# Optimization experiments

Hardware: AMD Instinct MI355X
Metric: run time of the kernel (lower is better)

The kernel has to match this reference:

```python
import jax, jax.numpy as jnp
import numpy as np

N_ATOMS = 100000
N_EDGES = 800000
ATOM_FDIM = 133
HIDDEN = 256
DEPTH = 3
NUM_MOLS = 4096
BN_EPS = 1e-5


def setup_inputs() -> dict:
    key = jax.random.key(0)
    ks = jax.random.split(key, 16)
    f_atoms = jax.random.normal(ks[0], (N_ATOMS, ATOM_FDIM), dtype=jnp.float32)
    edge_index = jax.random.randint(ks[1], (2, N_EDGES), 0, N_ATOMS, dtype=jnp.int64)
    segment_ids = jnp.sort(jax.random.randint(ks[2], (N_ATOMS,), 0, NUM_MOLS, dtype=jnp.int64))
    s = 1.0 / np.sqrt(HIDDEN)
    return {
        "f_atoms": f_atoms,
        "W_in_w": jax.random.normal(ks[3], (ATOM_FDIM, HIDDEN), dtype=jnp.float32) / np.sqrt(ATOM_FDIM),
        "W_in_b": jnp.zeros((HIDDEN,), dtype=jnp.float32),
        "w1": jax.random.normal(ks[4], (DEPTH, HIDDEN, HIDDEN), dtype=jnp.float32) * s,
        "b1": jnp.zeros((DEPTH, HIDDEN), dtype=jnp.float32),
        "g1": jnp.ones((DEPTH, HIDDEN), dtype=jnp.float32),
        "be1": jnp.zeros((DEPTH, HIDDEN), dtype=jnp.float32),
        "w2": jax.random.normal(ks[5], (DEPTH, HIDDEN, HIDDEN), dtype=jnp.float32) * s,
        "b2": jnp.zeros((DEPTH, HIDDEN), dtype=jnp.float32),
        "g2": jnp.ones((DEPTH, HIDDEN), dtype=jnp.float32),
        "be2": jnp.zeros((DEPTH, HIDDEN), dtype=jnp.float32),
        "eps": jnp.zeros((DEPTH,), dtype=jnp.float32),
        "edge_index": edge_index,
        "segment_ids": segment_ids,
    }


def batchnorm(h, gamma, beta):
    # BatchNorm1d with batch statistics over the node dimension (training-mode math)
    mean = jnp.mean(h, axis=0)
    var = jnp.var(h, axis=0)
    return (h - mean) * jax.lax.rsqrt(var + BN_EPS) * gamma + beta


def reference(f_atoms, W_in_w, W_in_b, w1, b1, g1, be1, w2, b2, g2, be2, eps,
              edge_index, segment_ids):
    src, dst = edge_index[0], edge_index[1]
    x = jax.nn.relu(f_atoms @ W_in_w + W_in_b)  # [N, H]
    for i in range(DEPTH):
        agg = jnp.zeros_like(x).at[dst].add(x[src])  # gather + scatter-add
        h = agg + (1.0 + eps[i]) * x                 # epsilon self-term
        h = jax.nn.relu(batchnorm(h @ w1[i] + b1[i], g1[i], be1[i]))
        h = jax.nn.relu(batchnorm(h @ w2[i] + b2[i], g2[i], be2[i]))
        x = h  # dropout = identity (eval)
    sums = jax.ops.segment_sum(x, segment_ids, num_segments=NUM_MOLS)
    counts = jax.ops.segment_sum(jnp.ones((x.shape[0],), x.dtype), segment_ids,
                                 num_segments=NUM_MOLS)
    return sums / jnp.maximum(counts, 1.0)[:, None]  # per-molecule mean
```

## Files before the change

kernel.cpp:

```cpp
#include <hip/hip_runtime.h>
#include <hip/hip_bf16.h>

#define NA 100000
#define NE 800000
#define FDIM 133
#define KIN 192
#define H 256
#define NMOL 4096

typedef __attribute__((ext_vector_type(8))) short s16x8;
typedef __attribute__((ext_vector_type(4))) float f32x4;
typedef __attribute__((ext_vector_type(4))) unsigned short u16x4;

__device__ __forceinline__ float bf2f(unsigned short h) {
    unsigned u = ((unsigned)h) << 16;
    return __builtin_bit_cast(float, u);
}
__device__ __forceinline__ unsigned short f2bf(float f) {
    unsigned u = __builtin_bit_cast(unsigned, f);
    u = u + 0x7FFFu + ((u >> 16) & 1u);
    return (unsigned short)(u >> 16);
}

__device__ __forceinline__ int swz(int row, int g) {
    return row * 64 + ((g ^ (row & 7)) << 3);
}

template<bool A_F32, bool AFFINE, bool RELU_OUT, bool STATS>
__global__ __launch_bounds__(256) void gemm_k(
    const void* __restrict__ Avoid,
    const unsigned short* __restrict__ BT,
    const float* __restrict__ bias,
    const float* __restrict__ aSc, const float* __restrict__ aSh,
    unsigned short* __restrict__ C,
    float* __restrict__ stSum, float* __restrict__ stSq,
    int M, int Kpad)
{
    __shared__ short lsA[128 * 64];
    __shared__ short lsB[128 * 64];
    __shared__ float lsSc[256], lsSh[256];
    __shared__ float lsS[128], lsQ[128];

    const int t = threadIdx.x;
    const int m0 = blockIdx.y * 128;
    const int n0 = blockIdx.x * 128;

    if (STATS && t < 128) { lsS[t] = 0.f; lsQ[t] = 0.f; }
    if (AFFINE) { lsSc[t] = aSc[t]; lsSh[t] = aSh[t]; }
    if (AFFINE) __syncthreads();

    const int sr = t >> 3;
    const int sg = t & 7;
    const int lane = t & 63;
    const int wid = t >> 6;
    const int wm = wid >> 1, wn = wid & 1;
    const int fr = lane & 15, fg = lane >> 4;

    f32x4 acc[4][4];
    #pragma unroll
    for (int i = 0; i < 4; i++)
        #pragma unroll
        for (int j = 0; j < 4; j++)
            acc[i][j] = f32x4{0.f, 0.f, 0.f, 0.f};

    const int nK = Kpad >> 6;
    s16x8 ra[4], rb[4];

    auto loadRegs = [&](int kc) {
        const int k0 = kc * 64;
        #pragma unroll
        for (int p = 0; p < 4; ++p) {
            int r = p * 32 + sr;
            int ga = m0 + r;
            if (A_F32) {
                const float* Af = (const float*)Avoid;
                s16x8 v;
                #pragma unroll
                for (int e = 0; e < 8; ++e) {
                    int k = k0 + sg * 8 + e;
                    float f = (ga < M && k < FDIM) ? Af[(size_t)ga * FDIM + k] : 0.f;
                    v[e] = (short)f2bf(f);
                }
                ra[p] = v;
            } else {
                const unsigned short* A = (const unsigned short*)Avoid;
                s16x8 z = {0,0,0,0,0,0,0,0};
                ra[p] = (ga < M) ? *(const s16x8*)(A + (size_t)ga * Kpad + k0 + sg * 8) : z;
            }
            rb[p] = *(const s16x8*)(BT + (size_t)(n0 + p * 32 + sr) * Kpad + k0 + sg * 8);
        }
    };
    auto writeLds = [&](int kc) {
        const int k0 = kc * 64;
        #pragma unroll
        for (int p = 0; p < 4; ++p) {
            int r = p * 32 + sr;
            s16x8 va = ra[p];
            if (AFFINE) {
                #pragma unroll
                for (int e = 0; e < 8; ++e) {
                    int k = k0 + sg * 8 + e;
                    float f = bf2f((unsigned short)va[e]);
                    f = fmaxf(f * lsSc[k] + lsSh[k], 0.f);
                    va[e] = (short)f2bf(f);
                }
            }
            *(s16x8*)&lsA[swz(r, sg)] = va;
            *(s16x8*)&lsB[swz(r, sg)] = rb[p];
        }
    };

    loadRegs(0);
    for (int kc = 0; kc < nK; ++kc) {
        writeLds(kc);
        __syncthreads();
        if (kc + 1 < nK) loadRegs(kc + 1);
        #pragma unroll
        for (int ks = 0; ks < 2; ++ks) {
            s16x8 af[4], bg[4];
            #pragma unroll
            for (int mi = 0; mi < 4; ++mi)
                af[mi] = *(const s16x8*)&lsA[swz(wm * 64 + mi * 16 + fr, ks * 4 + fg)];
            #pragma unroll
            for (int ni = 0; ni < 4; ++ni)
                bg[ni] = *(const s16x8*)&lsB[swz(wn * 64 + ni * 16 + fr, ks * 4 + fg)];
            #pragma unroll
            for (int mi = 0; mi < 4; ++mi)
                #pragma unroll
                for (int ni = 0; ni < 4; ++ni)
                    acc[mi][ni] = __builtin_amdgcn_mfma_f32_16x16x32_bf16(
                        af[mi], bg[ni], acc[mi][ni], 0, 0, 0);
        }
        __syncthreads();
    }

    float bc[4];
    #pragma unroll
    for (int ni = 0; ni < 4; ++ni)
        bc[ni] = bias[n0 + wn * 64 + ni * 16 + fr];
    float cs[4] = {0.f, 0.f, 0.f, 0.f}, cq[4] = {0.f, 0.f, 0.f, 0.f};
    #pragma unroll
    for (int mi = 0; mi < 4; ++mi) {
        #pragma unroll
        for (int r = 0; r < 4; ++r) {
            int row = m0 + wm * 64 + mi * 16 + fg * 4 + r;
            if (row < M) {
                #pragma unroll
                for (int ni = 0; ni < 4; ++ni) {
                    float v = acc[mi][ni][r] + bc[ni];
                    if (RELU_OUT) v = fmaxf(v, 0.f);
                    if (STATS) { cs[ni] += v; cq[ni] += v * v; }
                    C[(size_t)row * H + n0 + wn * 64 + ni * 16 + fr] = f2bf(v);
                }
            }
        }
    }
    if (STATS) {
        #pragma unroll
        for (int ni = 0; ni < 4; ++ni) {
            atomicAdd(&lsS[wn * 64 + ni * 16 + fr], cs[ni]);
            atomicAdd(&lsQ[wn * 64 + ni * 16 + fr], cq[ni]);
        }
        __syncthreads();
        if (t < 128) {
            atomicAdd(&stSum[n0 + t], lsS[t]);
            atomicAdd(&stSq[n0 + t], lsQ[t]);
        }
    }
}

__global__ void bnfin_k(float* __restrict__ sum, float* __restrict__ sumsq,
                        const float* __restrict__ g, const float* __restrict__ be,
                        float* __restrict__ scOut, float* __restrict__ shOut) {
    int c = threadIdx.x;
    float mean = sum[c] * (1.0f / NA);
    float var = sumsq[c] * (1.0f / NA) - mean * mean;
    float sc = g[c] * rsqrtf(var + 1e-5f);
    scOut[c] = sc;
    shOut[c] = be[c] - mean * sc;
    sum[c] = 0.f; sumsq[c] = 0.f;
}

__global__ void zero_k(int* __restrict__ counts, float* __restrict__ st) {
    int i = blockIdx.x * 256 + threadIdx.x;
    if (i < NA) counts[i] = 0;
    if (blockIdx.x == 0 && threadIdx.x < 256) { st[threadIdx.x] = 0.f; st[threadIdx.x + 256] = 0.f; }
}

__global__ void hist_k(const int* __restrict__ dst, int* __restrict__ counts) {
    int e = blockIdx.x * 256 + threadIdx.x;
    if (e < NE) atomicAdd(&counts[dst[e]], 1);
}
__global__ void scan1_k(const int* __restrict__ counts, int* __restrict__ excl, int* __restrict__ bsum) {
    __shared__ int sd[256];
    int i = blockIdx.x * 256 + threadIdx.x;
    int c = (i < NA) ? counts[i] : 0;
    sd[threadIdx.x] = c;
    __syncthreads();
    for (int off = 1; off < 256; off <<= 1) {
        int v = (threadIdx.x >= off) ? sd[threadIdx.x - off] : 0;
        __syncthreads();
        sd[threadIdx.x] += v;
        __syncthreads();
    }
    if (i < NA) excl[i] = sd[threadIdx.x] - c;
    if (threadIdx.x == 255) bsum[blockIdx.x] = sd[255];
}
__global__ void scan2_k(int* __restrict__ bsum, int nb) {
    __shared__ int sd[512];
    int t = threadIdx.x;
    int v = (t < nb) ? bsum[t] : 0;
    sd[t] = v;
    __syncthreads();
    for (int off = 1; off < 512; off <<= 1) {
        int u = (t >= off) ? sd[t - off] : 0;
        __syncthreads();
        sd[t] += u;
        __syncthreads();
    }
    if (t < nb) bsum[t] = sd[t] - v;
}
__global__ void scan3_k(int* __restrict__ rowstart, const int* __restrict__ bsum, int* __restrict__ cursor) {
    int i = blockIdx.x * 256 + threadIdx.x;
    if (i < NA) {
        int v = rowstart[i] + bsum[blockIdx.x];
        rowstart[i] = v;
        cursor[i] = v;
    }
}
__global__ void fill_k(const int* __restrict__ src, const int* __restrict__ dstArr,
                       int* __restrict__ cursor, int* __restrict__ esrc) {
    int e = blockIdx.x * 256 + threadIdx.x;
    if (e < NE) {
        int d = dstArr[e];
        int pos = atomicAdd(&cursor[d], 1);
        esrc[pos] = src[e];
    }
}

template<bool AFF>
__global__ __launch_bounds__(256) void agg_k(const unsigned short* __restrict__ X,
    const float* __restrict__ sc, const float* __restrict__ sh,
    const int* __restrict__ rowstart, const int* __restrict__ counts,
    const int* __restrict__ esrc, const float* __restrict__ epsArr, int layer,
    unsigned short* __restrict__ AGG)
{
    int wid = threadIdx.x >> 6, lane = threadIdx.x & 63;
    int row = blockIdx.x * 4 + wid;
    if (row >= NA) return;
    int half = lane >> 5;
    int c0 = (lane & 31) * 8;

    float s8[8], h8[8];
    if (AFF) {
        f32x4 a = *(const f32x4*)(sc + c0), b = *(const f32x4*)(sc + c0 + 4);
        f32x4 c = *(const f32x4*)(sh + c0), d = *(const f32x4*)(sh + c0 + 4);
        #pragma unroll
        for (int e = 0; e < 4; e++) { s8[e] = a[e]; s8[e + 4] = b[e]; h8[e] = c[e]; h8[e + 4] = d[e]; }
    }

    float a0[8] = {0,0,0,0,0,0,0,0}, a1[8] = {0,0,0,0,0,0,0,0};
    auto gath = [&](int i, float* a) {
        int sr2 = esrc[i];
        s16x8 u = *(const s16x8*)(X + (size_t)sr2 * H + c0);
        #pragma unroll
        for (int e = 0; e < 8; e++) {
            float f = bf2f((unsigned short)u[e]);
            if (AFF) f = fmaxf(f * s8[e] + h8[e], 0.f);
            a[e] += f;
        }
    };

    int s = rowstart[row], eEnd = s + counts[row];
    int i = s + half;
    for (; i + 2 < eEnd; i += 4) { gath(i, a0); gath(i + 2, a1); }
    if (i < eEnd) gath(i, a0);

    if (half == 0) {
        float e1 = 1.0f + epsArr[layer];
        s16x8 u = *(const s16x8*)(X + (size_t)row * H + c0);
        #pragma unroll
        for (int e = 0; e < 8; e++) {
            float f = bf2f((unsigned short)u[e]);
            if (AFF) f = fmaxf(f * s8[e] + h8[e], 0.f);
            a0[e] += f * e1;
        }
    }

    s16x8 o;
    #pragma unroll
    for (int e = 0; e < 8; e++) {
        float tot = a0[e] + a1[e];
        tot += __shfl_xor(tot, 32);
        o[e] = (short)f2bf(tot);
    }
    if (half == 0)
        *(s16x8*)(AGG + (size_t)row * H + c0) = o;
}

__global__ void prep_all_k(const float* __restrict__ Win, const float* __restrict__ w1,
                           const float* __restrict__ w2, unsigned short* __restrict__ BTall) {
    int i = blockIdx.x * 256 + threadIdx.x;
    const int NIN = 256 * KIN;
    if (i < NIN) {
        int n = i / KIN, k = i % KIN;
        BTall[i] = (k < FDIM) ? f2bf(Win[(size_t)k * 256 + n]) : (unsigned short)0;
    } else if (i < NIN + 6 * 65536) {
        int j = i - NIN;
        int d = j >> 16, r = j & 65535;
        int n = r >> 8, k = r & 255;
        const float* W = (d & 1) ? w2 : w1;
        BTall[i] = f2bf(W[(size_t)(d >> 1) * 65536 + (size_t)k * 256 + n]);
    }
}

__global__ void molstart_k(const int* __restrict__ seg, int* __restrict__ ms) {
    int m = blockIdx.x * 256 + threadIdx.x;
    if (m <= NMOL) {
        int lo = 0, hi = NA;
        while (lo < hi) { int mid = (lo + hi) >> 1; if (seg[mid] < m) lo = mid + 1; else hi = mid; }
        ms[m] = lo;
    }
}
__global__ __launch_bounds__(64) void mean_k(const unsigned short* __restrict__ X,
    const float* __restrict__ sc, const float* __restrict__ sh,
    const int* __restrict__ ms, float* __restrict__ out)
{
    int m = blockIdx.x, lane = threadIdx.x;
    int c0 = lane * 4;
    f32x4 s4 = *(const f32x4*)(sc + c0);
    f32x4 h4 = *(const f32x4*)(sh + c0);
    int a = ms[m], b = ms[m + 1];
    f32x4 acc{0.f, 0.f, 0.f, 0.f};
    for (int r = a; r < b; ++r) {
        u16x4 u = *(const u16x4*)(X + (size_t)r * H + c0);
        #pragma unroll
        for (int e = 0; e < 4; e++) acc[e] += fmaxf(bf2f(u[e]) * s4[e] + h4[e], 0.f);
    }
    float inv = (b > a) ? 1.0f / (float)(b - a) : 0.0f;
    #pragma unroll
    for (int e = 0; e < 4; e++) acc[e] *= inv;
    *(f32x4*)(out + (size_t)m * H + c0) = acc;
}

extern "C" void kernel_launch(void* const* d_in, const int* in_sizes, int n_in,
                              void* d_out, int out_size, void* d_ws, size_t ws_size,
                              hipStream_t stream) {
    const float* f_atoms = (const float*)d_in[0];
    const float* W_in_w  = (const float*)d_in[1];
    const float* W_in_b  = (const float*)d_in[2];
    const float* w1  = (const float*)d_in[3];
    const float* b1  = (const float*)d_in[4];
    const float* g1  = (const float*)d_in[5];
    const float* be1 = (const float*)d_in[6];
    const float* w2  = (const float*)d_in[7];
    const float* b2  = (const float*)d_in[8];
    const float* g2  = (const float*)d_in[9];
    const float* be2 = (const float*)d_in[10];
    const float* epsArr = (const float*)d_in[11];
    const int* edge = (const int*)d_in[12];
    const int* seg  = (const int*)d_in[13];
    float* out = (float*)d_out;

    char* w = (char*)d_ws;
    size_t off = 0;
    auto alloc = [&](size_t bytes) {
        char* p = w + off;
        off = (off + bytes + 255) & ~(size_t)255;
        return p;
    };
    unsigned short* X   = (unsigned short*)alloc((size_t)NA * H * 2);
    unsigned short* AGG = (unsigned short*)alloc((size_t)NA * H * 2);
    unsigned short* T1  = (unsigned short*)alloc((size_t)NA * H * 2);
    unsigned short* BTall = (unsigned short*)alloc(((size_t)256 * KIN + 6 * 65536) * 2);
    float* stSum = (float*)alloc(256 * 4);
    float* stSq  = (float*)alloc(256 * 4);
    float* sc1 = (float*)alloc(256 * 4);
    float* sh1 = (float*)alloc(256 * 4);
    float* sc2 = (float*)alloc(256 * 4);
    float* sh2 = (float*)alloc(256 * 4);
    int* counts   = (int*)alloc((size_t)NA * 4);
    int* rowstart = (int*)alloc((size_t)NA * 4);
    int* cursor   = (int*)alloc((size_t)NA * 4);
    int* esrc     = (int*)alloc((size_t)NE * 4);
    int* bsum     = (int*)alloc(512 * 4);
    int* ms       = (int*)alloc((NMOL + 1) * 4);

    unsigned short* BTin = BTall;
    unsigned short* BT1[3], *BT2[3];
    for (int d = 0; d < 3; ++d) {
        BT1[d] = BTall + 256 * KIN + (size_t)(2 * d) * 65536;
        BT2[d] = BTall + 256 * KIN + (size_t)(2 * d + 1) * 65536;
    }

    const int* esrcIn = edge;
    const int* edst   = edge + NE;

    zero_k<<<(NA + 255) / 256, 256, 0, stream>>>(counts, stSum);
    prep_all_k<<<(256 * KIN + 6 * 65536 + 255) / 256, 256, 0, stream>>>(W_in_w, w1, w2, BTall);

    hist_k<<<(NE + 255) / 256, 256, 0, stream>>>(edst, counts);
    scan1_k<<<391, 256, 0, stream>>>(counts, rowstart, bsum);
    scan2_k<<<1, 512, 0, stream>>>(bsum, 391);
    scan3_k<<<391, 256, 0, stream>>>(rowstart, bsum, cursor);
    fill_k<<<(NE + 255) / 256, 256, 0, stream>>>(esrcIn, edst, cursor, esrc);
    molstart_k<<<(NMOL + 256) / 256, 256, 0, stream>>>(seg, ms);

    gemm_k<true, false, true, false><<<dim3(2, (NA + 127) / 128), 256, 0, stream>>>(
        f_atoms, BTin, W_in_b, nullptr, nullptr, X, nullptr, nullptr, NA, KIN);

    for (int d = 0; d < 3; ++d) {
        if (d == 0)
            agg_k<false><<<(NA + 3) / 4, 256, 0, stream>>>(X, nullptr, nullptr,
                rowstart, counts, esrc, epsArr, d, AGG);
        else
            agg_k<true><<<(NA + 3) / 4, 256, 0, stream>>>(X, sc2, sh2,
                rowstart, counts, esrc, epsArr, d, AGG);
        gemm_k<false, false, false, true><<<dim3(2, (NA + 127) / 128), 256, 0, stream>>>(
            AGG, BT1[d], b1 + d * 256, nullptr, nullptr, T1, stSum, stSq, NA, 256);
        bnfin_k<<<1, 256, 0, stream>>>(stSum, stSq, g1 + d * 256, be1 + d * 256, sc1, sh1);
        gemm_k<false, true, false, true><<<dim3(2, (NA + 127) / 128), 256, 0, stream>>>(
            T1, BT2[d], b2 + d * 256, sc1, sh1, X, stSum, stSq, NA, 256);
        bnfin_k<<<1, 256, 0, stream>>>(stSum, stSq, g2 + d * 256, be2 + d * 256, sc2, sh2);
    }

    mean_k<<<NMOL, 64, 0, stream>>>(X, sc2, sh2, ms, out);
}
```

Before: 736.0 us.

## Double-buffer hidden GEMMs with direct global-to-LDS loads and fuse BN finalize

The hidden-layer GEMMs now stage A and B tiles straight into double-buffered LDS with global_load_lds, and apply the BN affine+ReLU on the LDS fragments instead of at staging time. A last-block ticket folds the BN finalize into the GEMM, which removes the separate bnfin launches. The input GEMM is split into its own kernel. The aggregation kernel uses a rowstart[N+1] CSR with split halves and 4-way unrolled gathers, and the molecule mean kernel uses 8-wide loads over two row halves. The risks are larger LDS use, which lowers occupancy, and correctness that depends on the ticket and threadfence ordering.

```diff
diff --git a/kernel.cpp b/kernel.cpp
--- a/kernel.cpp
+++ b/kernel.cpp
@@ -10,7 +10,6 @@
 
 typedef __attribute__((ext_vector_type(8))) short s16x8;
 typedef __attribute__((ext_vector_type(4))) float f32x4;
-typedef __attribute__((ext_vector_type(4))) unsigned short u16x4;
 
 __device__ __forceinline__ float bf2f(unsigned short h) {
     unsigned u = ((unsigned)h) << 16;
@@ -26,36 +25,53 @@
     return row * 64 + ((g ^ (row & 7)) << 3);
 }
 
-template<bool A_F32, bool AFFINE, bool RELU_OUT, bool STATS>
-__global__ __launch_bounds__(256) void gemm_k(
-    const void* __restrict__ Avoid,
+__device__ __forceinline__ void gload_lds16(const void* g, void* l) {
+    __builtin_amdgcn_global_load_lds((const __attribute__((address_space(1))) unsigned int*)g,
+                                     (__attribute__((address_space(3))) unsigned int*)l, 16, 0, 0);
+}
+
+template<bool AFFINE>
+__global__ __launch_bounds__(256) void gemmH_k(
+    const unsigned short* __restrict__ A,
     const unsigned short* __restrict__ BT,
     const float* __restrict__ bias,
     const float* __restrict__ aSc, const float* __restrict__ aSh,
     unsigned short* __restrict__ C,
-    float* __restrict__ stSum, float* __restrict__ stSq,
-    int M, int Kpad)
+    float* __restrict__ stSum, float* __restrict__ stSq, int* __restrict__ ticket,
+    const float* __restrict__ g, const float* __restrict__ be,
+    float* __restrict__ scOut, float* __restrict__ shOut,
+    int M)
 {
-    __shared__ short lsA[128 * 64];
-    __shared__ short lsB[128 * 64];
+    __shared__ short lsA2[2][128 * 64];
+    __shared__ short lsB2[2][128 * 64];
     __shared__ float lsSc[256], lsSh[256];
     __shared__ float lsS[128], lsQ[128];
+    __shared__ int lsLast;
 
     const int t = threadIdx.x;
     const int m0 = blockIdx.y * 128;
     const int n0 = blockIdx.x * 128;
 
-    if (STATS && t < 128) { lsS[t] = 0.f; lsQ[t] = 0.f; }
+    if (t < 128) { lsS[t] = 0.f; lsQ[t] = 0.f; }
     if (AFFINE) { lsSc[t] = aSc[t]; lsSh[t] = aSh[t]; }
-    if (AFFINE) __syncthreads();
-
-    const int sr = t >> 3;
-    const int sg = t & 7;
+
     const int lane = t & 63;
     const int wid = t >> 6;
     const int wm = wid >> 1, wn = wid & 1;
     const int fr = lane & 15, fg = lane >> 4;
 
+    auto stage = [&](int kc, int ab) {
+        #pragma unroll
+        for (int c = 0; c < 4; ++c) {
+            int slot = c * 256 + t;
+            int row = slot >> 3, gs = slot & 7;
+            int coff = kc * 64 + ((gs ^ (row & 7)) << 3);
+            if (m0 + row < M)
+                gload_lds16(A + (size_t)(m0 + row) * 256 + coff, &lsA2[ab][slot * 8]);
+            gload_lds16(BT + (size_t)(n0 + row) * 256 + coff, &lsB2[ab][slot * 8]);
+        }
+    };
+
     f32x4 acc[4][4];
     #pragma unroll
     for (int i = 0; i < 4; i++)
@@ -63,67 +79,38 @@
         for (int j = 0; j < 4; j++)
             acc[i][j] = f32x4{0.f, 0.f, 0.f, 0.f};
 
-    const int nK = Kpad >> 6;
-    s16x8 ra[4], rb[4];
-
-    auto loadRegs = [&](int kc) {
-        const int k0 = kc * 64;
-        #pragma unroll
-        for (int p = 0; p < 4; ++p) {
-            int r = p * 32 + sr;
-            int ga = m0 + r;
-            if (A_F32) {
-                const float* Af = (const float*)Avoid;
-                s16x8 v;
+    stage(0, 0);
+    __syncthreads();
+
+    for (int kc = 0; kc < 4; ++kc) {
+        int ab = kc & 1;
+        if (kc < 3) stage(kc + 1, ab ^ 1);
+        #pragma unroll
+        for (int ks = 0; ks < 2; ++ks) {
+            s16x8 af[4], bg[4];
+            #pragma unroll
+            for (int mi = 0; mi < 4; ++mi)
+                af[mi] = *(const s16x8*)&lsA2[ab][swz(wm * 64 + mi * 16 + fr, ks * 4 + fg)];
+            #pragma unroll
+            for (int ni = 0; ni < 4; ++ni)
+                bg[ni] = *(const s16x8*)&lsB2[ab][swz(wn * 64 + ni * 16 + fr, ks * 4 + fg)];
+            if (AFFINE) {
+                int kb = kc * 64 + ks * 32 + fg * 8;
+                f32x4 sA = *(const f32x4*)&lsSc[kb], sB = *(const f32x4*)&lsSc[kb + 4];
+                f32x4 hA = *(const f32x4*)&lsSh[kb], hB = *(const f32x4*)&lsSh[kb + 4];
                 #pragma unroll
-                for (int e = 0; e < 8; ++e) {
-                    int k = k0 + sg * 8 + e;
-                    float f = (ga < M && k < FDIM) ? Af[(size_t)ga * FDIM + k] : 0.f;
-                    v[e] = (short)f2bf(f);
-                }
-                ra[p] = v;
-            } else {
-                const unsigned short* A = (const unsigned short*)Avoid;
-                s16x8 z = {0,0,0,0,0,0,0,0};
-                ra[p] = (ga < M) ? *(const s16x8*)(A + (size_t)ga * Kpad + k0 + sg * 8) : z;
-            }
-            rb[p] = *(const s16x8*)(BT + (size_t)(n0 + p * 32 + sr) * Kpad + k0 + sg * 8);
-        }
-    };
-    auto writeLds = [&](int kc) {
-        const int k0 = kc * 64;
-        #pragma unroll
-        for (int p = 0; p < 4; ++p) {
-            int r = p * 32 + sr;
-            s16x8 va = ra[p];
-            if (AFFINE) {
-                #pragma unroll
-                for (int e = 0; e < 8; ++e) {
-                    int k = k0 + sg * 8 + e;
-                    float f = bf2f((unsigned short)va[e]);
-                    f = fmaxf(f * lsSc[k] + lsSh[k], 0.f);
-                    va[e] = (short)f2bf(f);
+                for (int mi = 0; mi < 4; ++mi) {
+                    s16x8 v = af[mi];
+                    #pragma unroll
+                    for (int e = 0; e < 4; ++e) {
+                        float f0 = fmaxf(bf2f((unsigned short)v[e]) * sA[e] + hA[e], 0.f);
+                        float f1 = fmaxf(bf2f((unsigned short)v[e + 4]) * sB[e] + hB[e], 0.f);
+                        v[e] = (short)f2bf(f0);
+                        v[e + 4] = (short)f2bf(f1);
+                    }
+                    af[mi] = v;
                 }
             }
-            *(s16x8*)&lsA[swz(r, sg)] = va;
-            *(s16x8*)&lsB[swz(r, sg)] = rb[p];
-        }
-    };
-
-    loadRegs(0);
-    for (int kc = 0; kc < nK; ++kc) {
-        writeLds(kc);
-        __syncthreads();
-        if (kc + 1 < nK) loadRegs(kc + 1);
-        #pragma unroll
-        for (int ks = 0; ks < 2; ++ks) {
-            s16x8 af[4], bg[4];
-            #pragma unroll
-            for (int mi = 0; mi < 4; ++mi)
-                af[mi] = *(const s16x8*)&lsA[swz(wm * 64 + mi * 16 + fr, ks * 4 + fg)];
-            #pragma unroll
-            for (int ni = 0; ni < 4; ++ni)
-                bg[ni] = *(const s16x8*)&lsB[swz(wn * 64 + ni * 16 + fr, ks * 4 + fg)];
             #pragma unroll
             for (int mi = 0; mi < 4; ++mi)
                 #pragma unroll
@@ -134,57 +121,150 @@
         __syncthreads();
     }
 
-    float bc[4];
     #pragma unroll
-    for (int ni = 0; ni < 4; ++ni)
-        bc[ni] = bias[n0 + wn * 64 + ni * 16 + fr];
-    float cs[4] = {0.f, 0.f, 0.f, 0.f}, cq[4] = {0.f, 0.f, 0.f, 0.f};
+    for (int ni = 0; ni < 4; ++ni) {
+        int lcol = wn * 64 + ni * 16 + fr;
+        float bc = bias[n0 + lcol];
+        float cs = 0.f, cq = 0.f;
+        #pragma unroll
+        for (int mi = 0; mi < 4; ++mi) {
+            #pragma unroll
+            for (int r = 0; r < 4; ++r) {
+                int row = m0 + wm * 64 + mi * 16 + fg * 4 + r;
+                if (row < M) {
+                    float v = acc[mi][ni][r] + bc;
+                    cs += v; cq += v * v;
+                    C[(size_t)row * H + n0 + lcol] = f2bf(v);
+                }
+            }
+        }
+        atomicAdd(&lsS[lcol], cs);
+        atomicAdd(&lsQ[lcol], cq);
+    }
+    __syncthreads();
+    if (t < 128) {
+        atomicAdd(&stSum[n0 + t], lsS[t]);
+        atomicAdd(&stSq[n0 + t], lsQ[t]);
+    }
+    __threadfence();
+    __syncthreads();
+    if (t == 0)
+        lsLast = (atomicAdd(ticket, 1) == (int)(gridDim.x * gridDim.y) - 1) ? 1 : 0;
+    __syncthreads();
+    if (lsLast) {
+        __threadfence();
+        if (t < 256) {
+            float mean = stSum[t] * (1.0f / (float)M);
+            float var = stSq[t] * (1.0f / (float)M) - mean * mean;
+            float sc = g[t] * rsqrtf(var + 1e-5f);
+            scOut[t] = sc;
+            shOut[t] = be[t] - mean * sc;
+            stSum[t] = 0.f; stSq[t] = 0.f;
+        }
+        if (t == 0) *ticket = 0;
+    }
+}
+
+__global__ __launch_bounds__(256) void gemmI_k(
+    const float* __restrict__ Af,
+    const unsigned short* __restrict__ BT,
+    const float* __restrict__ bias,
+    unsigned short* __restrict__ C, int M)
+{
+    __shared__ short lsA[128 * 64];
+    __shared__ short lsB[128 * 64];
+
+    const int t = threadIdx.x;
+    const int m0 = blockIdx.y * 128;
+    const int n0 = blockIdx.x * 128;
+    const int sr = t >> 3, sg = t & 7;
+    const int lane = t & 63, wid = t >> 6;
+    const int wm = wid >> 1, wn = wid & 1;
+    const int fr = lane & 15, fg = lane >> 4;
+
+    f32x4 acc[4][4];
     #pragma unroll
-    for (int mi = 0; mi < 4; ++mi) {
-        #pragma unroll
-        for (int r = 0; r < 4; ++r) {
-            int row = m0 + wm * 64 + mi * 16 + fg * 4 + r;
-            if (row < M) {
+    for (int i = 0; i < 4; i++)
+        #pragma unroll
+        for (int j = 0; j < 4; j++)
+            acc[i][j] = f32x4{0.f, 0.f, 0.f, 0.f};
+
+    s16x8 ra[4], rb[4];
+    auto loadRegs = [&](int kc) {
+        const int k0 = kc * 64;
+        #pragma unroll
+        for (int p = 0; p < 4; ++p) {
+            int r = p * 32 + sr;
+            int ga = m0 + r;
+            s16x8 v;
+            #pragma unroll
+            for (int e = 0; e < 8; ++e) {
+                int k = k0 + sg * 8 + e;
+                float f = (ga < M && k < FDIM) ? Af[(size_t)ga * FDIM + k] : 0.f;
+                v[e] = (short)f2bf(f);
+            }
+            ra[p] = v;
+            rb[p] = *(const s16x8*)(BT + (size_t)(n0 + r) * KIN + k0 + sg * 8);
+        }
+    };
+    auto writeLds = [&]() {
+        #pragma unroll
+        for (int p = 0; p < 4; ++p) {
+            int r = p * 32 + sr;
+            *(s16x8*)&lsA[swz(r, sg)] = ra[p];
+            *(s16x8*)&lsB[swz(r, sg)] = rb[p];
+        }
+    };
+
+    loadRegs(0);
+    for (int kc = 0; kc < 3; ++kc) {
+        writeLds();
+        __syncthreads();
+        if (kc + 1 < 3) loadRegs(kc + 1);
+        #pragma unroll
+        for (int ks = 0; ks < 2; ++ks) {
+            s16x8 af[4], bg[4];
+            #pragma unroll
+            for (int mi = 0; mi < 4; ++mi)
+                af[mi] = *(const s16x8*)&lsA[swz(wm * 64 + mi * 16 + fr, ks * 4 + fg)];
+            #pragma unroll
+            for (int ni = 0; ni < 4; ++ni)
+                bg[ni] = *(const s16x8*)&lsB[swz(wn * 64 + ni * 16 + fr, ks * 4 + fg)];
+            #pragma unroll
+            for (int mi = 0; mi < 4; ++mi)
                 #pragma unroll
-                for (int ni = 0; ni < 4; ++ni) {
-                    float v = acc[mi][ni][r] + bc[ni];
-                    if (RELU_OUT) v = fmaxf(v, 0.f);
-                    if (STATS) { cs[ni] += v; cq[ni] += v * v; }
+                for (int ni = 0; ni < 4; ++ni)
+                    acc[mi][ni] = __builtin_amdgcn_mfma_f32_16x16x32_bf16(
+                        af[mi], bg[ni], acc[mi][ni], 0, 0, 0);
+        }
+        __syncthreads();
+    }
+
+    #pragma unroll
+    for (int ni = 0; ni < 4; ++ni) {
+        float bc = bias[n0 + wn * 64 + ni * 16 + fr];
+        #pragma unroll
+        for (int mi = 0; mi < 4; ++mi) {
+            #pragma unroll
+            for (int r = 0; r < 4; ++r) {
+                int row = m0 + wm * 64 + mi * 16 + fg * 4 + r;
+                if (row < M) {
+                    float v = fmaxf(acc[mi][ni][r] + bc, 0.f);
                     C[(size_t)row * H + n0 + wn * 64 + ni * 16 + fr] = f2bf(v);
                 }
             }
         }
     }
-    if (STATS) {
-        #pragma unroll
-        for (int ni = 0; ni < 4; ++ni) {
-            atomicAdd(&lsS[wn * 64 + ni * 16 + fr], cs[ni]);
-            atomicAdd(&lsQ[wn * 64 + ni * 16 + fr], cq[ni]);
-        }
-        __syncthreads();
-        if (t < 128) {
-            atomicAdd(&stSum[n0 + t], lsS[t]);
-            atomicAdd(&stSq[n0 + t], lsQ[t]);
-        }
-    }
-}
-
-__global__ void bnfin_k(float* __restrict__ sum, float* __restrict__ sumsq,
-                        const float* __restrict__ g, const float* __restrict__ be,
-                        float* __restrict__ scOut, float* __restrict__ shOut) {
-    int c = threadIdx.x;
-    float mean = sum[c] * (1.0f / NA);
-    float var = sumsq[c] * (1.0f / NA) - mean * mean;
-    float sc = g[c] * rsqrtf(var + 1e-5f);
-    scOut[c] = sc;
-    shOut[c] = be[c] - mean * sc;
-    sum[c] = 0.f; sumsq[c] = 0.f;
-}
-
-__global__ void zero_k(int* __restrict__ counts, float* __restrict__ st) {
+}
+
+__global__ void zero_k(int* __restrict__ counts, float* __restrict__ st,
+                       int* __restrict__ ticket, int* __restrict__ rowstart) {
     int i = blockIdx.x * 256 + threadIdx.x;
     if (i < NA) counts[i] = 0;
-    if (blockIdx.x == 0 && threadIdx.x < 256) { st[threadIdx.x] = 0.f; st[threadIdx.x + 256] = 0.f; }
+    if (blockIdx.x == 0) {
+        st[threadIdx.x] = 0.f; st[threadIdx.x + 256] = 0.f;
+        if (threadIdx.x == 0) { *ticket = 0; rowstart[NA] = NE; }
+    }
 }
 
 __global__ void hist_k(const int* __restrict__ dst, int* __restrict__ counts) {
@@ -241,13 +321,12 @@
 template<bool AFF>
 __global__ __launch_bounds__(256) void agg_k(const unsigned short* __restrict__ X,
     const float* __restrict__ sc, const float* __restrict__ sh,
-    const int* __restrict__ rowstart, const int* __restrict__ counts,
+    const int* __restrict__ rowstart,
     const int* __restrict__ esrc, const float* __restrict__ epsArr, int layer,
     unsigned short* __restrict__ AGG)
 {
     int wid = threadIdx.x >> 6, lane = threadIdx.x & 63;
     int row = blockIdx.x * 4 + wid;
-    if (row >= NA) return;
     int half = lane >> 5;
     int c0 = (lane & 31) * 8;
 
@@ -260,9 +339,7 @@
     }
 
     float a0[8] = {0,0,0,0,0,0,0,0}, a1[8] = {0,0,0,0,0,0,0,0};
-    auto gath = [&](int i, float* a) {
-        int sr2 = esrc[i];
-        s16x8 u = *(const s16x8*)(X + (size_t)sr2 * H + c0);
+    auto addv = [&](s16x8 u, float* a) {
         #pragma unroll
         for (int e = 0; e < 8; e++) {
             float f = bf2f((unsigned short)u[e]);
@@ -271,10 +348,23 @@
         }
     };
 
-    int s = rowstart[row], eEnd = s + counts[row];
-    int i = s + half;
-    for (; i + 2 < eEnd; i += 4) { gath(i, a0); gath(i + 2, a1); }
-    if (i < eEnd) gath(i, a0);
+    int s = rowstart[row], eEnd = rowstart[row + 1];
+    int cnt = eEnd - s, mid = s + (cnt >> 1);
+    int i = half ? mid : s;
+    int end = half ? eEnd : mid;
+    for (; i + 3 < end; i += 4) {
+        int e0 = esrc[i], e1 = esrc[i + 1], e2 = esrc[i + 2], e3 = esrc[i + 3];
+        s16x8 u0 = *(const s16x8*)(X + (size_t)e0 * H + c0);
+        s16x8 u1 = *(const s16x8*)(X + (size_t)e1 * H + c0);
+        s16x8 u2 = *(const s16x8*)(X + (size_t)e2 * H + c0);
+        s16x8 u3 = *(const s16x8*)(X + (size_t)e3 * H + c0);
+        addv(u0, a0); addv(u1, a1); addv(u2, a0); addv(u3, a1);
+    }
+    for (; i < end; ++i) {
+        int e0 = esrc[i];
+        s16x8 u = *(const s16x8*)(X + (size_t)e0 * H + c0);
+        addv(u, a0);
+    }
 
     if (half == 0) {
         float e1 = 1.0f + epsArr[layer];
@@ -327,20 +417,35 @@
     const int* __restrict__ ms, float* __restrict__ out)
 {
     int m = blockIdx.x, lane = threadIdx.x;
-    int c0 = lane * 4;
-    f32x4 s4 = *(const f32x4*)(sc + c0);
-    f32x4 h4 = *(const f32x4*)(sh + c0);
+    int half = lane >> 5;
+    int c0 = (lane & 31) * 8;
+    float s8[8], h8[8];
+    {
+        f32x4 a = *(const f32x4*)(sc + c0), b = *(const f32x4*)(sc + c0 + 4);
+        f32x4 c = *(const f32x4*)(sh + c0), d = *(const f32x4*)(sh + c0 + 4);
+        #pragma unroll
+        for (int e = 0; e < 4; e++) { s8[e] = a[e]; s8[e + 4] = b[e]; h8[e] = c[e]; h8[e + 4] = d[e]; }
+    }
     int a = ms[m], b = ms[m + 1];
-    f32x4 acc{0.f, 0.f, 0.f, 0.f};
-    for (int r = a; r < b; ++r) {
-        u16x4 u = *(const u16x4*)(X + (size_t)r * H + c0);
-        #pragma unroll
-        for (int e = 0; e < 4; e++) acc[e] += fmaxf(bf2f(u[e]) * s4[e] + h4[e], 0.f);
+    float acc[8] = {0,0,0,0,0,0,0,0};
+    for (int r = a + half; r < b; r += 2) {
+        s16x8 u = *(const s16x8*)(X + (size_t)r * H + c0);
+        #pragma unroll
+        for (int e = 0; e < 8; e++)
+            acc[e] += fmaxf(bf2f((unsigned short)u[e]) * s8[e] + h8[e], 0.f);
     }
     float inv = (b > a) ? 1.0f / (float)(b - a) : 0.0f;
+    f32x4 o0, o1;
     #pragma unroll
-    for (int e = 0; e < 4; e++) acc[e] *= inv;
-    *(f32x4*)(out + (size_t)m * H + c0) = acc;
+    for (int e = 0; e < 8; e++) {
+        float tot = acc[e] + __shfl_xor(acc[e], 32);
+        tot *= inv;
+        if (e < 4) o0[e] = tot; else o1[e - 4] = tot;
+    }
+    if (half == 0) {
+        *(f32x4*)(out + (size_t)m * H + c0) = o0;
+        *(f32x4*)(out + (size_t)m * H + c0 + 4) = o1;
+    }
 }
 
 extern "C" void kernel_launch(void* const* d_in, const int* in_sizes, int n_in,
@@ -380,11 +485,12 @@
     float* sc2 = (float*)alloc(256 * 4);
     float* sh2 = (float*)alloc(256 * 4);
     int* counts   = (int*)alloc((size_t)NA * 4);
-    int* rowstart = (int*)alloc((size_t)NA * 4);
+    int* rowstart = (int*)alloc((size_t)(NA + 1) * 4);
     int* cursor   = (int*)alloc((size_t)NA * 4);
     int* esrc     = (int*)alloc((size_t)NE * 4);
     int* bsum     = (int*)alloc(512 * 4);
     int* ms       = (int*)alloc((NMOL + 1) * 4);
+    int* ticket   = (int*)alloc(256);
 
     unsigned short* BTin = BTall;
     unsigned short* BT1[3], *BT2[3];
@@ -396,7 +502,7 @@
     const int* esrcIn = edge;
     const int* edst   = edge + NE;
 
-    zero_k<<<(NA + 255) / 256, 256, 0, stream>>>(counts, stSum);
+    zero_k<<<(NA + 255) / 256, 256, 0, stream>>>(counts, stSum, ticket, rowstart);
     prep_all_k<<<(256 * KIN + 6 * 65536 + 255) / 256, 256, 0, stream>>>(W_in_w, w1, w2, BTall);
 
     hist_k<<<(NE + 255) / 256, 256, 0, stream>>>(edst, counts);
@@ -406,22 +512,21 @@
     fill_k<<<(NE + 255) / 256, 256, 0, stream>>>(esrcIn, edst, cursor, esrc);
     molstart_k<<<(NMOL + 256) / 256, 256, 0, stream>>>(seg, ms);
 
-    gemm_k<true, false, true, false><<<dim3(2, (NA + 127) / 128), 256, 0, stream>>>(
-        f_atoms, BTin, W_in_b, nullptr, nullptr, X, nullptr, nullptr, NA, KIN);
+    gemmI_k<<<dim3(2, (NA + 127) / 128), 256, 0, stream>>>(f_atoms, BTin, W_in_b, X, NA);
 
     for (int d = 0; d < 3; ++d) {
         if (d == 0)
-            agg_k<false><<<(NA + 3) / 4, 256, 0, stream>>>(X, nullptr, nullptr,
-                rowstart, counts, esrc, epsArr, d, AGG);
+            agg_k<false><<<NA / 4, 256, 0, stream>>>(X, nullptr, nullptr,
+                rowstart, esrc, epsArr, d, AGG);
         else
-            agg_k<true><<<(NA + 3) / 4, 256, 0, stream>>>(X, sc2, sh2,
-                rowstart, counts, esrc, epsArr, d, AGG);
-        gemm_k<false, false, false, true><<<dim3(2, (NA + 127) / 128), 256, 0, stream>>>(
-            AGG, BT1[d], b1 + d * 256, nullptr, nullptr, T1, stSum, stSq, NA, 256);
-        bnfin_k<<<1, 256, 0, stream>>>(stSum, stSq, g1 + d * 256, be1 + d * 256, sc1, sh1);
-        gemm_k<false, true, false, true><<<dim3(2, (NA + 127) / 128), 256, 0, stream>>>(
-            T1, BT2[d], b2 + d * 256, sc1, sh1, X, stSum, stSq, NA, 256);
-        bnfin_k<<<1, 256, 0, stream>>>(stSum, stSq, g2 + d * 256, be2 + d * 256, sc2, sh2);
+            agg_k<true><<<NA / 4, 256, 0, stream>>>(X, sc2, sh2,
+                rowstart, esrc, epsArr, d, AGG);
+        gemmH_k<false><<<dim3(2, (NA + 127) / 128), 256, 0, stream>>>(
+            AGG, BT1[d], b1 + d * 256, nullptr, nullptr, T1,
+            stSum, stSq, ticket, g1 + d * 256, be1 + d * 256, sc1, sh1, NA);
+        gemmH_k<true><<<dim3(2, (NA + 127) / 128), 256, 0, stream>>>(
+            T1, BT2[d], b2 + d * 256, sc1, sh1, X,
+            stSum, stSq, ticket, g2 + d * 256, be2 + d * 256, sc2, sh2, NA);
     }
 
     mean_k<<<NMOL, 64, 0, stream>>>(X, sc2, sh2, ms, out);
```

After: 1.717 ms. 133% more time.
